# Optimization experiments

Hardware: AMD Instinct MI355X
Metric: run time of the kernel (lower is better)

Reference implementation:

```python
import jax, jax.numpy as jnp
import numpy as np
import math

B, NQ, NKV, D, H, KP = 4, 8192, 8192, 256, 8, 256
HD = D // H


def setup_inputs() -> dict:
    key = jax.random.key(0)
    ks = jax.random.split(key, 8)
    s = 1.0 / math.sqrt(D)
    return {
        "x1": jax.random.normal(ks[0], (B, NQ, D), dtype=jnp.float32),
        "x2": jax.random.normal(ks[1], (NKV, D), dtype=jnp.float32),
        "Wq": jax.random.normal(ks[2], (D, D), dtype=jnp.float32) * s,
        "Wk": jax.random.normal(ks[3], (D, D), dtype=jnp.float32) * s,
        "Wv": jax.random.normal(ks[4], (D, D), dtype=jnp.float32) * s,
        "Wo": jax.random.normal(ks[5], (D, D), dtype=jnp.float32) * s,
        "E": jax.random.normal(ks[6], (NKV, KP), dtype=jnp.float32) * (1.0 / math.sqrt(NKV)),
        "F": jax.random.normal(ks[7], (NKV, KP), dtype=jnp.float32) * (1.0 / math.sqrt(NKV)),
    }


def reference(x1, x2, Wq, Wk, Wv, Wo, E, F):
    # x1: [B, NQ, D] queries; x2: [NKV, D] shared cross-attention context
    q = x1 @ Wq                               # [B, NQ, D]
    k = x2 @ Wk                               # [NKV, D]
    v = x2 @ Wv                               # [NKV, D]
    # Linformer low-rank compression along the KV sequence axis
    k_low = jnp.einsum('nd,nk->kd', k, E)     # [KP, D]
    v_low = jnp.einsum('nd,nk->kd', v, F)     # [KP, D]
    qh = q.reshape(B, NQ, H, HD)
    kh = k_low.reshape(KP, H, HD)
    vh = v_low.reshape(KP, H, HD)
    scale = 1.0 / math.sqrt(HD)
    scores = jnp.einsum('bqhd,khd->bhqk', qh, kh) * scale  # [B, H, NQ, KP]
    attn = jax.nn.softmax(scores, axis=-1)
    out = jnp.einsum('bhqk,khd->bqhd', attn, vh)           # [B, NQ, H, HD]
    out = out.reshape(B, NQ, D)
    return out @ Wo
```

## Files before the change

kernel.cpp:

```cpp
#include <hip/hip_runtime.h>
#include <math.h>
#include <stdint.h>


typedef unsigned short ushort_t;
typedef __attribute__((ext_vector_type(8))) short bf16x8;
typedef __attribute__((ext_vector_type(8))) _Float16 f16x8;
typedef __attribute__((ext_vector_type(4))) float f32x4;

__device__ __forceinline__ f32x4 MFMA(bf16x8 a, bf16x8 b, f32x4 c) {
  return __builtin_amdgcn_mfma_f32_16x16x32_bf16(a, b, c, 0, 0, 0);
}
__device__ __forceinline__ f32x4 MFMA_H(f16x8 a, f16x8 b, f32x4 c) {
  return __builtin_amdgcn_mfma_f32_16x16x32_f16(a, b, c, 0, 0, 0);
}
__device__ __forceinline__ ushort_t f2bf(float x) {
  uint32_t u = __float_as_uint(x);
  u += 0x7fffu + ((u >> 16) & 1u);
  return (ushort_t)(u >> 16);
}
#define GLDS(gsrc, ldst)                                                    \
  __builtin_amdgcn_global_load_lds(                                         \
      (const __attribute__((address_space(1))) uint32_t*)(const void*)(gsrc), \
      (__attribute__((address_space(3))) uint32_t*)(void*)(ldst), 16, 0, 0)

#define STAGE_ROW(u) \
  (((((u) >> 2) ^ ((u) >> 4)) & 1) | (((u) >> 2) & 6) | (((u) >> 5) << 3))
#define STAGE_G(u) \
  ((((u) ^ ((u) >> 2) ^ ((u) >> 4)) & 1) | (((((u) >> 1) ^ ((u) >> 3)) & 1) << 1))

__global__ __launch_bounds__(256) void k_transpose(
    const float* __restrict__ x2, const float* __restrict__ E,
    const float* __restrict__ F, _Float16* __restrict__ xt) {
  __shared__ float tile[64][65];
  const int t = threadIdx.x;
  const int n0 = blockIdx.x * 64;
  const int c0 = blockIdx.y * 64;
  const int z = blockIdx.z;
  const float* __restrict__ src = (z == 0) ? x2 : (z == 1) ? E : F;
  _Float16* __restrict__ dst = xt + (size_t)z * 2097152;
  const int rr = t >> 4, cc = (t & 15) * 4;
#pragma unroll
  for (int i = 0; i < 4; ++i) {
    float4 v = *(const float4*)&src[(size_t)(n0 + rr + 16 * i) * 256 + c0 + cc];
    tile[cc + 0][rr + 16 * i] = v.x;
    tile[cc + 1][rr + 16 * i] = v.y;
    tile[cc + 2][rr + 16 * i] = v.z;
    tile[cc + 3][rr + 16 * i] = v.w;
  }
  __syncthreads();
#pragma unroll
  for (int rnd = 0; rnd < 2; ++rnd) {
    const int u = rnd * 256 + t;
    const int c = u >> 3, r0 = (u & 7) * 8;
    f16x8 h;
#pragma unroll
    for (int j = 0; j < 8; ++j) h[j] = (_Float16)tile[c][r0 + j];
    *(f16x8*)&dst[(size_t)(c0 + c) * 8192 + n0 + r0] = h;
  }
}

__global__ __launch_bounds__(256) void k_prep_w(
    const float* __restrict__ Wq, const float* __restrict__ Wk,
    const float* __restrict__ Wv, const float* __restrict__ Wo,
    ushort_t* __restrict__ wqt, ushort_t* __restrict__ wot,
    _Float16* __restrict__ wkt, _Float16* __restrict__ wvt) {
  const int id = blockIdx.x * 256 + threadIdx.x;
  const int task = blockIdx.y;
  const int n = id >> 8, k = id & 255;
  if (task == 0) wqt[id] = f2bf(Wq[k * 256 + n] * 0.25503488f);
  else if (task == 1) wot[id] = f2bf(Wo[k * 256 + n]);
  else if (task == 2) wkt[id] = (_Float16)Wk[k * 256 + n];
  else wvt[id] = (_Float16)Wv[k * 256 + n];
}

__global__ __launch_bounds__(256, 2) void k_etx2_mfma(
    const _Float16* __restrict__ xt, float* __restrict__ part) {
  __shared__ __align__(16) _Float16 ab[2][2][8192];
  const int t = threadIdx.x;
  const int ln = t & 63;
  const int wv = t >> 6;
  const int l15 = ln & 15, g = ln >> 4;
  const int wr = wv >> 1, wc = wv & 1;
  const int kp0 = (blockIdx.x >> 1) * 128;
  const int d0 = (blockIdx.x & 1) * 128;
  const int chunk = blockIdx.y;
  const int which = blockIdx.z;
  const int n0 = chunk * 256;
  const _Float16* __restrict__ A = xt + (size_t)(1 + which) * 2097152;
  const _Float16* __restrict__ B = xt;

  auto stage = [&](int buf, int ks) {
#pragma unroll
    for (int m = 0; m < 2; ++m)
#pragma unroll
      for (int rnd = 0; rnd < 4; ++rnd) {
        const int u = rnd * 256 + t;
        const int row = u >> 3;
        const int cb = (u & 7) << 4;
        const int csw = cb ^ ((row & 7) << 4);
        const _Float16* gs =
            (m ? B + (size_t)(d0 + row) * 8192 : A + (size_t)(kp0 + row) * 8192) +
            n0 + ks * 64 + (csw >> 1);
        GLDS(gs, (char*)&ab[buf][m][0] + (u & ~63) * 16);
      }
  };

  f32x4 acc[4][4];
#pragma unroll
  for (int i = 0; i < 4; ++i)
#pragma unroll
    for (int j = 0; j < 4; ++j) acc[i][j] = {0.f, 0.f, 0.f, 0.f};

  stage(0, 0);
  __syncthreads();
  for (int ks = 0; ks < 4; ++ks) {
    if (ks < 3) stage((ks + 1) & 1, ks + 1);
    const char* la = (const char*)&ab[ks & 1][0][0];
    const char* lb = (const char*)&ab[ks & 1][1][0];
#pragma unroll
    for (int kk = 0; kk < 2; ++kk) {
      f16x8 af[4], bf[4];
#pragma unroll
      for (int i = 0; i < 4; ++i) {
        const int ra = wr * 64 + i * 16 + l15;
        af[i] = *(const f16x8*)(la + ra * 128 +
                                ((kk * 64 + g * 16) ^ ((ra & 7) << 4)));
      }
#pragma unroll
      for (int j = 0; j < 4; ++j) {
        const int rb = wc * 64 + j * 16 + l15;
        bf[j] = *(const f16x8*)(lb + rb * 128 +
                                ((kk * 64 + g * 16) ^ ((rb & 7) << 4)));
      }
#pragma unroll
      for (int i = 0; i < 4; ++i)
#pragma unroll
        for (int j = 0; j < 4; ++j) acc[i][j] = MFMA_H(af[i], bf[j], acc[i][j]);
    }
    __syncthreads();
  }
  float* __restrict__ p = part + ((size_t)which * 32 + chunk) * 65536;
#pragma unroll
  for (int i = 0; i < 4; ++i)
#pragma unroll
    for (int j = 0; j < 4; ++j)
#pragma unroll
      for (int r = 0; r < 4; ++r)
        p[(size_t)(kp0 + wr * 64 + i * 16 + g * 4 + r) * 256 + d0 + wc * 64 +
          j * 16 + l15] = acc[i][j][r];
}

__global__ __launch_bounds__(256) void k_reduce_part(
    const float* __restrict__ part, _Float16* __restrict__ ghh) {
  const int oid = blockIdx.x * 256 + threadIdx.x;
  const int which = oid >> 16;
  const int base = oid & 65535;
  const float* __restrict__ p = part + (size_t)which * 32 * 65536 + base;
  float s = 0.f;
#pragma unroll
  for (int c = 0; c < 32; ++c) s += p[c * 65536];
  ghh[oid] = (_Float16)s;
}

__global__ __launch_bounds__(256, 4) void k_lowproj(
    const _Float16* __restrict__ ghh, const _Float16* __restrict__ wkt,
    const _Float16* __restrict__ wvt, float* __restrict__ kvlow) {
  __shared__ __align__(16) _Float16 wstage[2][4096];
  const int t = threadIdx.x;
  const int wv = t >> 6, ln = t & 63;
  const int l15 = ln & 15, g = ln >> 4;
  const int which = blockIdx.y;
  const size_t r0 = (size_t)blockIdx.x * 64;
  const _Float16* __restrict__ A = ghh + (size_t)which * 65536;
  const _Float16* __restrict__ W = which ? wvt : wkt;
  float* __restrict__ outp = kvlow + (size_t)which * 65536;

  auto stage = [&](int row0, int colu, int buf) {
#pragma unroll
    for (int rnd = 0; rnd < 2; ++rnd) {
      const int u = rnd * 256 + wv * 64 + ln;
      const int row = STAGE_ROW(u);
      const int gg = STAGE_G(u);
      GLDS(W + (size_t)(row0 + row) * 256 + colu + gg * 8,
           &wstage[buf][(rnd * 256 + wv * 64) * 8]);
    }
  };

  f32x4 yacc[16];
#pragma unroll
  for (int i = 0; i < 16; ++i) yacc[i] = {0.f, 0.f, 0.f, 0.f};
  stage(0, 0, 0);
  const _Float16* arow = A + (r0 + wv * 16 + l15) * 256;
  __syncthreads();
  for (int ci = 0; ci < 16; ++ci) {
    const int nh = ci & 1, ks = ci >> 1;
    if (ci < 15) stage(((ci + 1) & 1) * 128, ((ci + 1) >> 1) * 32, (ci + 1) & 1);
    f16x8 afrag = *(const f16x8*)(arow + ks * 32 + g * 8);
    const _Float16* cw = wstage[ci & 1];
#pragma unroll
    for (int tt = 0; tt < 8; ++tt) {
      f16x8 bfr = *(const f16x8*)&cw[((tt * 16 + l15) * 32 + g * 8) ^
                                     ((l15 & 7) << 3)];
      yacc[nh * 8 + tt] = MFMA_H(afrag, bfr, yacc[nh * 8 + tt]);
    }
    __syncthreads();
  }
#pragma unroll
  for (int tt = 0; tt < 16; ++tt)
#pragma unroll
    for (int r = 0; r < 4; ++r)
      outp[(r0 + wv * 16 + g * 4 + r) * 256 + tt * 16 + l15] = yacc[tt][r];
}

__global__ __launch_bounds__(256) void k_prep2(
    const float* __restrict__ kvlow, ushort_t* __restrict__ klowA,
    ushort_t* __restrict__ vtb) {
  const int id = blockIdx.x * 256 + threadIdx.x;
  if (blockIdx.y == 0) {
    const int h = id >> 13, kp = (id >> 5) & 255, d = id & 31;
    klowA[h * 8192 + (((kp << 5) | d) ^ ((kp & 7) << 3))] =
        f2bf(kvlow[kp * 256 + h * 32 + d]);
  } else {
    const int kl = id & 127, d = (id >> 7) & 31, kh = (id >> 12) & 1, h = id >> 13;
    vtb[(((h * 2 + kh) * 32 + d) << 7) + (kl ^ ((d & 7) << 3))] =
        f2bf(kvlow[65536 + (kh * 128 + kl) * 256 + h * 32 + d]);
  }
}

__global__ __launch_bounds__(256, 4) void k_qgemm(
    const float* __restrict__ x1, const ushort_t* __restrict__ wqt,
    ushort_t* __restrict__ Qf) {
  __shared__ __align__(16) char smem[32768];
  const int t = threadIdx.x;
  const int wv = t >> 6, ln = t & 63;
  const int l15 = ln & 15, g = ln >> 4;
  const size_t r0 = (size_t)blockIdx.x * 64;
  ushort_t* wstage = (ushort_t*)smem;

  auto stage = [&](int row0, int colu, int buf) {
#pragma unroll
    for (int rnd = 0; rnd < 2; ++rnd) {
      const int u = rnd * 256 + wv * 64 + ln;
      const int row = STAGE_ROW(u);
      const int gg = STAGE_G(u);
      GLDS(wqt + (size_t)(row0 + row) * 256 + colu + gg * 8,
           &wstage[buf * 4096 + (rnd * 256 + wv * 64) * 8]);
    }
  };

  f32x4 qacc[16];
#pragma unroll
  for (int i = 0; i < 16; ++i) qacc[i] = {0.f, 0.f, 0.f, 0.f};
  stage(0, 0, 0);
  const float* xrow = x1 + (r0 + wv * 16 + l15) * 256;
  float4 xa = *(const float4*)(xrow + g * 8);
  float4 xb = *(const float4*)(xrow + g * 8 + 4);
  __syncthreads();

  for (int ci = 0; ci < 16; ++ci) {
    const int nh = ci & 1;
    if (ci < 15) stage(((ci + 1) & 1) * 128, ((ci + 1) >> 1) * 32, (ci + 1) & 1);
    bf16x8 afrag;
    afrag[0] = (short)f2bf(xa.x); afrag[1] = (short)f2bf(xa.y);
    afrag[2] = (short)f2bf(xa.z); afrag[3] = (short)f2bf(xa.w);
    afrag[4] = (short)f2bf(xb.x); afrag[5] = (short)f2bf(xb.y);
    afrag[6] = (short)f2bf(xb.z); afrag[7] = (short)f2bf(xb.w);
    const ushort_t* cw = &wstage[(ci & 1) * 4096];
#pragma unroll
    for (int tt = 0; tt < 8; ++tt) {
      bf16x8 bfr = *(const bf16x8*)&cw[((tt * 16 + l15) * 32 + g * 8) ^
                                       ((l15 & 7) << 3)];
      qacc[nh * 8 + tt] = MFMA(afrag, bfr, qacc[nh * 8 + tt]);
    }
    if (nh == 1 && ci < 15) {
      int ks = (ci >> 1) + 1;
      xa = *(const float4*)(xrow + ks * 32 + g * 8);
      xb = *(const float4*)(xrow + ks * 32 + g * 8 + 4);
    }
    __syncthreads();
  }
  char* myq = smem + wv * 8192;
#pragma unroll
  for (int tt = 0; tt < 16; ++tt)
#pragma unroll
    for (int r = 0; r < 4; ++r) {
      const int gr = g * 4 + r;
      *(ushort_t*)(myq + gr * 512 + (((tt * 16 + l15) * 2) ^ ((gr & 7) << 4))) =
          f2bf(qacc[tt][r]);
    }
  __builtin_amdgcn_sched_barrier(0);
  const int rt = blockIdx.x * 4 + wv;
#pragma unroll
  for (int hh = 0; hh < 8; ++hh) {
    bf16x8 qf = *(const bf16x8*)(myq + l15 * 512 +
                                 ((hh * 64 + g * 16) ^ ((l15 & 7) << 4)));
    *(bf16x8*)&Qf[((size_t)(rt * 8 + hh) * 64 + ln) * 8] = qf;
  }
}

__global__ __launch_bounds__(512, 4) void k_attn(
    const ushort_t* __restrict__ Qf, const ushort_t* __restrict__ klowA,
    const ushort_t* __restrict__ vtb, ushort_t* __restrict__ O) {
  __shared__ __align__(16) ushort_t kv[16384];
  __shared__ __align__(16) uint32_t p_buf[8][320];
  __shared__ __align__(16) ushort_t o_sl[8][640];
  const int t = threadIdx.x;
  const int wv = t >> 6, ln = t & 63;
  const int l15 = ln & 15, g = ln >> 4;
  const int h = blockIdx.y;
  const size_t r0 = (size_t)blockIdx.x * 128;

  {
    const ushort_t* ksrc = klowA + h * 8192;
    const ushort_t* vsrc = vtb + h * 8192;
#pragma unroll
    for (int rnd = 0; rnd < 2; ++rnd) {
      const int ub = rnd * 512 + wv * 64;
      GLDS(ksrc + (ub + ln) * 8, &kv[ub * 8]);
    }
#pragma unroll
    for (int rnd = 0; rnd < 2; ++rnd) {
      const int ub = rnd * 512 + wv * 64;
      GLDS(vsrc + (ub + ln) * 8, &kv[8192 + ub * 8]);
    }
  }
  const int rt = blockIdx.x * 8 + wv;
  bf16x8 qfrag = *(const bf16x8*)&Qf[((size_t)(rt * 8 + h) * 64 + ln) * 8];
  __syncthreads();

  f32x4 s[16];
#pragma unroll
  for (int tt = 0; tt < 16; ++tt) {
    bf16x8 kfr = *(const bf16x8*)&kv[((tt * 16 + l15) * 32 + g * 8) ^
                                     ((l15 & 7) << 3)];
    f32x4 z = {0.f, 0.f, 0.f, 0.f};
    s[tt] = MFMA(kfr, qfrag, z);
  }
  float sum = 0.f;
  uint32_t pw[16][2];
#pragma unroll
  for (int tt = 0; tt < 16; ++tt) {
    float e0 = exp2f(s[tt][0]), e1 = exp2f(s[tt][1]);
    float e2 = exp2f(s[tt][2]), e3 = exp2f(s[tt][3]);
    sum += (e0 + e1) + (e2 + e3);
    pw[tt][0] = (uint32_t)f2bf(e0) | ((uint32_t)f2bf(e1) << 16);
    pw[tt][1] = (uint32_t)f2bf(e2) | ((uint32_t)f2bf(e3) << 16);
  }
  sum += __shfl_xor(sum, 16);
  sum += __shfl_xor(sum, 32);
  const float rinv = 1.0f / sum;
  float rv[4];
#pragma unroll
  for (int r = 0; r < 4; ++r) rv[r] = __shfl(rinv, g * 4 + r);

  f32x4 oacc[2];
  oacc[0] = {0.f, 0.f, 0.f, 0.f};
  oacc[1] = {0.f, 0.f, 0.f, 0.f};
  uint32_t* pbw = &p_buf[wv][l15 * 20];
#pragma unroll
  for (int kh = 0; kh < 2; ++kh) {
    const char* cv = (const char*)&kv[8192 + kh * 4096];
#pragma unroll
    for (int ksl = 0; ksl < 4; ++ksl) {
      const int ks = kh * 4 + ksl;
      pbw[2 * g + 0] = pw[2 * ks][0];
      pbw[2 * g + 1] = pw[2 * ks][1];
      pbw[8 + 2 * g + 0] = pw[2 * ks + 1][0];
      pbw[8 + 2 * g + 1] = pw[2 * ks + 1][1];
      __builtin_amdgcn_sched_barrier(0);
      bf16x8 pfr = *(const bf16x8*)&p_buf[wv][l15 * 20 + 4 * g];
#pragma unroll
      for (int nt = 0; nt < 2; ++nt) {
        bf16x8 vfr = *(const bf16x8*)(cv + (nt * 16 + l15) * 256 +
                                      ((ksl * 64 + g * 16) ^ ((l15 & 7) << 4)));
        oacc[nt] = MFMA(pfr, vfr, oacc[nt]);
      }
      __builtin_amdgcn_sched_barrier(0);
    }
  }
#pragma unroll
  for (int nt = 0; nt < 2; ++nt)
#pragma unroll
    for (int r = 0; r < 4; ++r)
      o_sl[wv][(g * 4 + r) * 40 + nt * 16 + l15] = f2bf(oacc[nt][r] * rv[r]);
  __builtin_amdgcn_sched_barrier(0);
  {
    const int qr = ln >> 2, d0 = (ln & 3) * 8;
    bf16x8 ov = *(const bf16x8*)&o_sl[wv][qr * 40 + d0];
    *(bf16x8*)&O[(r0 + wv * 16 + qr) * 256 + h * 32 + d0] = ov;
  }
}

__global__ __launch_bounds__(256, 4) void k_ogemm(
    const ushort_t* __restrict__ O, const ushort_t* __restrict__ wot,
    float* __restrict__ out) {
  __shared__ __align__(16) ushort_t wstage[2][4096];
  const int t = threadIdx.x;
  const int wv = t >> 6, ln = t & 63;
  const int l15 = ln & 15, g = ln >> 4;
  const size_t r0 = (size_t)blockIdx.x * 64;

  auto stage = [&](int row0, int colu, int buf) {
#pragma unroll
    for (int rnd = 0; rnd < 2; ++rnd) {
      const int u = rnd * 256 + wv * 64 + ln;
      const int row = STAGE_ROW(u);
      const int gg = STAGE_G(u);
      GLDS(wot + (size_t)(row0 + row) * 256 + colu + gg * 8,
           &wstage[buf][(rnd * 256 + wv * 64) * 8]);
    }
  };

  f32x4 yacc[16];
#pragma unroll
  for (int i = 0; i < 16; ++i) yacc[i] = {0.f, 0.f, 0.f, 0.f};
  stage(0, 0, 0);
  const ushort_t* arow = O + (r0 + wv * 16 + l15) * 256;
  __syncthreads();
  for (int ci = 0; ci < 16; ++ci) {
    const int nh = ci & 1, ks = ci >> 1;
    if (ci < 15) stage(((ci + 1) & 1) * 128, ((ci + 1) >> 1) * 32, (ci + 1) & 1);
    bf16x8 afrag = *(const bf16x8*)(arow + ks * 32 + g * 8);
    const ushort_t* cw = wstage[ci & 1];
#pragma unroll
    for (int tt = 0; tt < 8; ++tt) {
      bf16x8 bfr = *(const bf16x8*)&cw[((tt * 16 + l15) * 32 + g * 8) ^
                                       ((l15 & 7) << 3)];
      yacc[nh * 8 + tt] = MFMA(afrag, bfr, yacc[nh * 8 + tt]);
    }
    __syncthreads();
  }
#pragma unroll
  for (int tt = 0; tt < 16; ++tt)
#pragma unroll
    for (int r = 0; r < 4; ++r)
      out[(r0 + wv * 16 + g * 4 + r) * 256 + tt * 16 + l15] = yacc[tt][r];
}

extern "C" void kernel_launch(void* const* d_in, const int* in_sizes, int n_in,
                              void* d_out, int out_size, void* d_ws, size_t ws_size,
                              hipStream_t stream) {
  const float* x1 = (const float*)d_in[0];
  const float* x2 = (const float*)d_in[1];
  const float* Wq = (const float*)d_in[2];
  const float* Wk = (const float*)d_in[3];
  const float* Wv = (const float*)d_in[4];
  const float* Wo = (const float*)d_in[5];
  const float* E  = (const float*)d_in[6];
  const float* F  = (const float*)d_in[7];
  float* out = (float*)d_out;
  float* ws = (float*)d_ws;
  _Float16* ghh = (_Float16*)ws;
  float* kvlow = ws + 65536;
  ushort_t* wqt = (ushort_t*)(ws + 196608);
  ushort_t* wot = (ushort_t*)(ws + 229376);
  _Float16* wkt = (_Float16*)(ws + 262144);
  _Float16* wvt = (_Float16*)(ws + 294912);
  ushort_t* klowA = (ushort_t*)(ws + 327680);
  ushort_t* vtb = (ushort_t*)(ws + 360448);
  float* part = ws + 393216;
  ushort_t* Qf = (ushort_t*)(ws + 393216);
  _Float16* xt = (_Float16*)(ws + 4587520);
  ushort_t* O = (ushort_t*)(ws + 4587520);

  k_transpose<<<dim3(128, 4, 3), 256, 0, stream>>>(x2, E, F, xt);
  k_prep_w<<<dim3(256, 4), 256, 0, stream>>>(Wq, Wk, Wv, Wo, wqt, wot, wkt, wvt);
  k_etx2_mfma<<<dim3(4, 32, 2), 256, 0, stream>>>(xt, part);
  k_reduce_part<<<512, 256, 0, stream>>>(part, ghh);
  k_lowproj<<<dim3(4, 2), 256, 0, stream>>>(ghh, wkt, wvt, kvlow);
  k_prep2<<<dim3(256, 2), 256, 0, stream>>>(kvlow, klowA, vtb);
  k_qgemm<<<512, 256, 0, stream>>>(x1, wqt, Qf);
  k_attn<<<dim3(256, 8), 512, 0, stream>>>(Qf, klowA, vtb, O);
  k_ogemm<<<512, 256, 0, stream>>>(O, wot, out);
}
```

Baseline: 98.81 us.

## Merge prep kernels, co-schedule Q GEMM with E^T x2 GEMM, fuse low-proj repack

Merges the x2/E/F transpose and the weight transposes into one launch, and transposes the weights through LDS tiles for coalesced access. The Q projection and the E^T·x2 / F^T·x2 partial GEMMs now run as separate block ranges of a single kernel, so their work overlaps. The partial GEMM uses larger K chunks, which halves the reduction partials, but it loses double buffering. The low-rank projection writes the swizzled bf16 K/V layouts directly, removing the prep2 kernel and the fp32 intermediate. The attention kernel handles two query tiles per block. Fewer launches and overlapped independent work are the aim; the risk is slower per-block pipelining in the partial GEMM.

```diff
diff --git a/kernel.cpp b/kernel.cpp
--- a/kernel.cpp
+++ b/kernel.cpp
@@ -29,126 +29,215 @@
 #define STAGE_G(u) \
   ((((u) ^ ((u) >> 2) ^ ((u) >> 4)) & 1) | (((((u) >> 1) ^ ((u) >> 3)) & 1) << 1))
 
-__global__ __launch_bounds__(256) void k_transpose(
+__global__ __launch_bounds__(256) void k_prep_all(
     const float* __restrict__ x2, const float* __restrict__ E,
-    const float* __restrict__ F, _Float16* __restrict__ xt) {
+    const float* __restrict__ F, const float* __restrict__ Wq,
+    const float* __restrict__ Wk, const float* __restrict__ Wv,
+    const float* __restrict__ Wo, _Float16* __restrict__ xt,
+    ushort_t* __restrict__ wqt, ushort_t* __restrict__ wot,
+    _Float16* __restrict__ wkt, _Float16* __restrict__ wvt) {
   __shared__ float tile[64][65];
   const int t = threadIdx.x;
-  const int n0 = blockIdx.x * 64;
-  const int c0 = blockIdx.y * 64;
   const int z = blockIdx.z;
-  const float* __restrict__ src = (z == 0) ? x2 : (z == 1) ? E : F;
-  _Float16* __restrict__ dst = xt + (size_t)z * 2097152;
-  const int rr = t >> 4, cc = (t & 15) * 4;
-#pragma unroll
-  for (int i = 0; i < 4; ++i) {
-    float4 v = *(const float4*)&src[(size_t)(n0 + rr + 16 * i) * 256 + c0 + cc];
-    tile[cc + 0][rr + 16 * i] = v.x;
-    tile[cc + 1][rr + 16 * i] = v.y;
-    tile[cc + 2][rr + 16 * i] = v.z;
-    tile[cc + 3][rr + 16 * i] = v.w;
-  }
-  __syncthreads();
-#pragma unroll
-  for (int rnd = 0; rnd < 2; ++rnd) {
-    const int u = rnd * 256 + t;
-    const int c = u >> 3, r0 = (u & 7) * 8;
-    f16x8 h;
-#pragma unroll
-    for (int j = 0; j < 8; ++j) h[j] = (_Float16)tile[c][r0 + j];
-    *(f16x8*)&dst[(size_t)(c0 + c) * 8192 + n0 + r0] = h;
-  }
-}
-
-__global__ __launch_bounds__(256) void k_prep_w(
-    const float* __restrict__ Wq, const float* __restrict__ Wk,
-    const float* __restrict__ Wv, const float* __restrict__ Wo,
-    ushort_t* __restrict__ wqt, ushort_t* __restrict__ wot,
-    _Float16* __restrict__ wkt, _Float16* __restrict__ wvt) {
-  const int id = blockIdx.x * 256 + threadIdx.x;
-  const int task = blockIdx.y;
-  const int n = id >> 8, k = id & 255;
-  if (task == 0) wqt[id] = f2bf(Wq[k * 256 + n] * 0.25503488f);
-  else if (task == 1) wot[id] = f2bf(Wo[k * 256 + n]);
-  else if (task == 2) wkt[id] = (_Float16)Wk[k * 256 + n];
-  else wvt[id] = (_Float16)Wv[k * 256 + n];
-}
-
-__global__ __launch_bounds__(256, 2) void k_etx2_mfma(
-    const _Float16* __restrict__ xt, float* __restrict__ part) {
-  __shared__ __align__(16) _Float16 ab[2][2][8192];
+  if (z < 3) {
+    const int n0 = blockIdx.x * 64;
+    const int c0 = blockIdx.y * 64;
+    const float* __restrict__ src = (z == 0) ? x2 : (z == 1) ? E : F;
+    _Float16* __restrict__ dst = xt + (size_t)z * 2097152;
+    const int rr = t >> 4, cc = (t & 15) * 4;
+#pragma unroll
+    for (int i = 0; i < 4; ++i) {
+      float4 v = *(const float4*)&src[(size_t)(n0 + rr + 16 * i) * 256 + c0 + cc];
+      tile[cc + 0][rr + 16 * i] = v.x;
+      tile[cc + 1][rr + 16 * i] = v.y;
+      tile[cc + 2][rr + 16 * i] = v.z;
+      tile[cc + 3][rr + 16 * i] = v.w;
+    }
+    __syncthreads();
+#pragma unroll
+    for (int rnd = 0; rnd < 2; ++rnd) {
+      const int u = rnd * 256 + t;
+      const int c = u >> 3, r0 = (u & 7) * 8;
+      f16x8 h;
+#pragma unroll
+      for (int j = 0; j < 8; ++j) h[j] = (_Float16)tile[c][r0 + j];
+      *(f16x8*)&dst[(size_t)(c0 + c) * 8192 + n0 + r0] = h;
+    }
+  } else {
+    if (blockIdx.x >= 16) return;
+    const int m = blockIdx.y;
+    const float* __restrict__ src = (m == 0) ? Wq : (m == 1) ? Wo
+                                  : (m == 2) ? Wk : Wv;
+    const int tr = (blockIdx.x >> 2) * 64;
+    const int tc = (blockIdx.x & 3) * 64;
+    const int rr = t >> 4, cc = (t & 15) * 4;
+#pragma unroll
+    for (int i = 0; i < 4; ++i) {
+      float4 v = *(const float4*)&src[(size_t)(tr + rr + 16 * i) * 256 + tc + cc];
+      tile[cc + 0][rr + 16 * i] = v.x;
+      tile[cc + 1][rr + 16 * i] = v.y;
+      tile[cc + 2][rr + 16 * i] = v.z;
+      tile[cc + 3][rr + 16 * i] = v.w;
+    }
+    __syncthreads();
+#pragma unroll
+    for (int rnd = 0; rnd < 2; ++rnd) {
+      const int u = rnd * 256 + t;
+      const int nl = u >> 3, kl = (u & 7) * 8;
+      if (m < 2) {
+        const float sc = (m == 0) ? 0.25503488f : 1.0f;
+        bf16x8 hv;
+#pragma unroll
+        for (int j = 0; j < 8; ++j) hv[j] = (short)f2bf(tile[nl][kl + j] * sc);
+        ushort_t* dst = (m == 0) ? wqt : wot;
+        *(bf16x8*)&dst[(size_t)(tc + nl) * 256 + tr + kl] = hv;
+      } else {
+        f16x8 hv;
+#pragma unroll
+        for (int j = 0; j < 8; ++j) hv[j] = (_Float16)tile[nl][kl + j];
+        _Float16* dst = (m == 2) ? wkt : wvt;
+        *(f16x8*)&dst[(size_t)(tc + nl) * 256 + tr + kl] = hv;
+      }
+    }
+  }
+}
+
+__global__ __launch_bounds__(256, 3) void k_mega1(
+    const float* __restrict__ x1, const _Float16* __restrict__ xt,
+    const ushort_t* __restrict__ wqt, ushort_t* __restrict__ Qf,
+    float* __restrict__ part) {
+  __shared__ __align__(16) char smem[32768];
   const int t = threadIdx.x;
-  const int ln = t & 63;
-  const int wv = t >> 6;
+  const int wv = t >> 6, ln = t & 63;
   const int l15 = ln & 15, g = ln >> 4;
-  const int wr = wv >> 1, wc = wv & 1;
-  const int kp0 = (blockIdx.x >> 1) * 128;
-  const int d0 = (blockIdx.x & 1) * 128;
-  const int chunk = blockIdx.y;
-  const int which = blockIdx.z;
-  const int n0 = chunk * 256;
-  const _Float16* __restrict__ A = xt + (size_t)(1 + which) * 2097152;
-  const _Float16* __restrict__ B = xt;
-
-  auto stage = [&](int buf, int ks) {
-#pragma unroll
-    for (int m = 0; m < 2; ++m)
-#pragma unroll
-      for (int rnd = 0; rnd < 4; ++rnd) {
-        const int u = rnd * 256 + t;
-        const int row = u >> 3;
-        const int cb = (u & 7) << 4;
-        const int csw = cb ^ ((row & 7) << 4);
+
+  if (blockIdx.x < 512) {
+    ushort_t* wstage = (ushort_t*)smem;
+    const size_t r0 = (size_t)blockIdx.x * 64;
+    auto stage = [&](int row0, int colu, int buf) {
+#pragma unroll
+      for (int rnd = 0; rnd < 2; ++rnd) {
+        const int u = rnd * 256 + wv * 64 + ln;
+        const int row = STAGE_ROW(u);
+        const int gg = STAGE_G(u);
+        GLDS(wqt + (size_t)(row0 + row) * 256 + colu + gg * 8,
+             &wstage[(buf * 512 + rnd * 256 + wv * 64) * 8]);
+      }
+    };
+    f32x4 qacc[16];
+#pragma unroll
+    for (int i = 0; i < 16; ++i) qacc[i] = {0.f, 0.f, 0.f, 0.f};
+    stage(0, 0, 0);
+    const float* xrow = x1 + (r0 + wv * 16 + l15) * 256;
+    float4 xa = *(const float4*)(xrow + g * 8);
+    float4 xb = *(const float4*)(xrow + g * 8 + 4);
+    __syncthreads();
+    for (int ci = 0; ci < 16; ++ci) {
+      const int nh = ci & 1;
+      if (ci < 15) stage(((ci + 1) & 1) * 128, ((ci + 1) >> 1) * 32, (ci + 1) & 1);
+      bf16x8 afrag;
+      afrag[0] = (short)f2bf(xa.x); afrag[1] = (short)f2bf(xa.y);
+      afrag[2] = (short)f2bf(xa.z); afrag[3] = (short)f2bf(xa.w);
+      afrag[4] = (short)f2bf(xb.x); afrag[5] = (short)f2bf(xb.y);
+      afrag[6] = (short)f2bf(xb.z); afrag[7] = (short)f2bf(xb.w);
+      const ushort_t* cw = &wstage[(ci & 1) * 4096];
+#pragma unroll
+      for (int tt = 0; tt < 8; ++tt) {
+        bf16x8 bfr = *(const bf16x8*)&cw[((tt * 16 + l15) * 32 + g * 8) ^
+                                         ((l15 & 7) << 3)];
+        qacc[nh * 8 + tt] = MFMA(afrag, bfr, qacc[nh * 8 + tt]);
+      }
+      if (nh == 1 && ci < 15) {
+        int ks = (ci >> 1) + 1;
+        xa = *(const float4*)(xrow + ks * 32 + g * 8);
+        xb = *(const float4*)(xrow + ks * 32 + g * 8 + 4);
+      }
+      __syncthreads();
+    }
+    char* myq = smem + wv * 8192;
+#pragma unroll
+    for (int tt = 0; tt < 16; ++tt)
+#pragma unroll
+      for (int r = 0; r < 4; ++r) {
+        const int gr = g * 4 + r;
+        *(ushort_t*)(myq + gr * 512 + (((tt * 16 + l15) * 2) ^ ((gr & 7) << 4))) =
+            f2bf(qacc[tt][r]);
+      }
+    __builtin_amdgcn_sched_barrier(0);
+    const int rt = blockIdx.x * 4 + wv;
+#pragma unroll
+    for (int hh = 0; hh < 8; ++hh) {
+      bf16x8 qf = *(const bf16x8*)(myq + l15 * 512 +
+                                   ((hh * 64 + g * 16) ^ ((l15 & 7) << 4)));
+      *(bf16x8*)&Qf[((size_t)(rt * 8 + hh) * 64 + ln) * 8] = qf;
+    }
+  } else {
+    const int bid = blockIdx.x - 512;
+    const int which = bid & 1;
+    const int chunk = (bid >> 1) & 15;
+    const int quad = bid >> 5;
+    const int kp0 = (quad >> 1) * 128;
+    const int d0 = (quad & 1) * 128;
+    const int n0 = chunk * 512;
+    const _Float16* __restrict__ A = xt + (size_t)(1 + which) * 2097152;
+    const _Float16* __restrict__ B = xt;
+    const int wr = wv >> 1, wc = wv & 1;
+    f32x4 acc[4][4];
+#pragma unroll
+    for (int i = 0; i < 4; ++i)
+#pragma unroll
+      for (int j = 0; j < 4; ++j) acc[i][j] = {0.f, 0.f, 0.f, 0.f};
+
+    for (int ks = 0; ks < 8; ++ks) {
+#pragma unroll
+      for (int r8 = 0; r8 < 8; ++r8) {
+        const int u = r8 * 256 + t;
+        const int mm = u >> 10;
+        const int uu = u & 1023;
+        const int row = uu >> 3;
+        const int nsw = ((uu ^ row) & 7) << 3;
         const _Float16* gs =
-            (m ? B + (size_t)(d0 + row) * 8192 : A + (size_t)(kp0 + row) * 8192) +
-            n0 + ks * 64 + (csw >> 1);
-        GLDS(gs, (char*)&ab[buf][m][0] + (u & ~63) * 16);
-      }
-  };
-
-  f32x4 acc[4][4];
-#pragma unroll
-  for (int i = 0; i < 4; ++i)
-#pragma unroll
-    for (int j = 0; j < 4; ++j) acc[i][j] = {0.f, 0.f, 0.f, 0.f};
-
-  stage(0, 0);
-  __syncthreads();
-  for (int ks = 0; ks < 4; ++ks) {
-    if (ks < 3) stage((ks + 1) & 1, ks + 1);
-    const char* la = (const char*)&ab[ks & 1][0][0];
-    const char* lb = (const char*)&ab[ks & 1][1][0];
-#pragma unroll
-    for (int kk = 0; kk < 2; ++kk) {
-      f16x8 af[4], bf[4];
-#pragma unroll
-      for (int i = 0; i < 4; ++i) {
-        const int ra = wr * 64 + i * 16 + l15;
-        af[i] = *(const f16x8*)(la + ra * 128 +
-                                ((kk * 64 + g * 16) ^ ((ra & 7) << 4)));
-      }
-#pragma unroll
-      for (int j = 0; j < 4; ++j) {
-        const int rb = wc * 64 + j * 16 + l15;
-        bf[j] = *(const f16x8*)(lb + rb * 128 +
-                                ((kk * 64 + g * 16) ^ ((rb & 7) << 4)));
-      }
-#pragma unroll
-      for (int i = 0; i < 4; ++i)
-#pragma unroll
-        for (int j = 0; j < 4; ++j) acc[i][j] = MFMA_H(af[i], bf[j], acc[i][j]);
-    }
-    __syncthreads();
-  }
-  float* __restrict__ p = part + ((size_t)which * 32 + chunk) * 65536;
-#pragma unroll
-  for (int i = 0; i < 4; ++i)
-#pragma unroll
-    for (int j = 0; j < 4; ++j)
-#pragma unroll
-      for (int r = 0; r < 4; ++r)
-        p[(size_t)(kp0 + wr * 64 + i * 16 + g * 4 + r) * 256 + d0 + wc * 64 +
-          j * 16 + l15] = acc[i][j][r];
+            (mm ? B + (size_t)(d0 + row) * 8192
+                : A + (size_t)(kp0 + row) * 8192) +
+            n0 + ks * 64 + nsw;
+        GLDS(gs, smem + (u & ~63) * 16);
+      }
+      __syncthreads();
+      const char* la = smem;
+      const char* lb = smem + 16384;
+#pragma unroll
+      for (int kk = 0; kk < 2; ++kk) {
+        f16x8 af[4], bf[4];
+#pragma unroll
+        for (int i = 0; i < 4; ++i) {
+          const int ra = wr * 64 + i * 16 + l15;
+          af[i] = *(const f16x8*)(la + ra * 128 +
+                                  ((kk * 64 + g * 16) ^ ((ra & 7) << 4)));
+        }
+#pragma unroll
+        for (int j = 0; j < 4; ++j) {
+          const int rb = wc * 64 + j * 16 + l15;
+          bf[j] = *(const f16x8*)(lb + rb * 128 +
+                                  ((kk * 64 + g * 16) ^ ((rb & 7) << 4)));
+        }
+#pragma unroll
+        for (int i = 0; i < 4; ++i)
+#pragma unroll
+          for (int j = 0; j < 4; ++j)
+            acc[i][j] = MFMA_H(af[i], bf[j], acc[i][j]);
+      }
+      __syncthreads();
+    }
+    float* __restrict__ p = part + ((size_t)which * 16 + chunk) * 65536;
+#pragma unroll
+    for (int i = 0; i < 4; ++i)
+#pragma unroll
+      for (int j = 0; j < 4; ++j)
+#pragma unroll
+        for (int r = 0; r < 4; ++r)
+          p[(size_t)(kp0 + wr * 64 + i * 16 + g * 4 + r) * 256 + d0 + wc * 64 +
+            j * 16 + l15] = acc[i][j][r];
+  }
 }
 
 __global__ __launch_bounds__(256) void k_reduce_part(
@@ -156,25 +245,25 @@
   const int oid = blockIdx.x * 256 + threadIdx.x;
   const int which = oid >> 16;
   const int base = oid & 65535;
-  const float* __restrict__ p = part + (size_t)which * 32 * 65536 + base;
+  const float* __restrict__ p = part + (size_t)which * 16 * 65536 + base;
   float s = 0.f;
 #pragma unroll
-  for (int c = 0; c < 32; ++c) s += p[c * 65536];
+  for (int c = 0; c < 16; ++c) s += p[c * 65536];
   ghh[oid] = (_Float16)s;
 }
 
-__global__ __launch_bounds__(256, 4) void k_lowproj(
+__global__ __launch_bounds__(256, 4) void k_lowproj2(
     const _Float16* __restrict__ ghh, const _Float16* __restrict__ wkt,
-    const _Float16* __restrict__ wvt, float* __restrict__ kvlow) {
+    const _Float16* __restrict__ wvt, ushort_t* __restrict__ klowA,
+    ushort_t* __restrict__ vtb) {
   __shared__ __align__(16) _Float16 wstage[2][4096];
   const int t = threadIdx.x;
   const int wv = t >> 6, ln = t & 63;
   const int l15 = ln & 15, g = ln >> 4;
   const int which = blockIdx.y;
-  const size_t r0 = (size_t)blockIdx.x * 64;
+  const int r0 = blockIdx.x * 64;
   const _Float16* __restrict__ A = ghh + (size_t)which * 65536;
   const _Float16* __restrict__ W = which ? wvt : wkt;
-  float* __restrict__ outp = kvlow + (size_t)which * 65536;
 
   auto stage = [&](int row0, int colu, int buf) {
 #pragma unroll
@@ -191,7 +280,7 @@
 #pragma unroll
   for (int i = 0; i < 16; ++i) yacc[i] = {0.f, 0.f, 0.f, 0.f};
   stage(0, 0, 0);
-  const _Float16* arow = A + (r0 + wv * 16 + l15) * 256;
+  const _Float16* arow = A + (size_t)(r0 + wv * 16 + l15) * 256;
   __syncthreads();
   for (int ci = 0; ci < 16; ++ci) {
     const int nh = ci & 1, ks = ci >> 1;
@@ -209,94 +298,18 @@
 #pragma unroll
   for (int tt = 0; tt < 16; ++tt)
 #pragma unroll
-    for (int r = 0; r < 4; ++r)
-      outp[(r0 + wv * 16 + g * 4 + r) * 256 + tt * 16 + l15] = yacc[tt][r];
-}
-
-__global__ __launch_bounds__(256) void k_prep2(
-    const float* __restrict__ kvlow, ushort_t* __restrict__ klowA,
-    ushort_t* __restrict__ vtb) {
-  const int id = blockIdx.x * 256 + threadIdx.x;
-  if (blockIdx.y == 0) {
-    const int h = id >> 13, kp = (id >> 5) & 255, d = id & 31;
-    klowA[h * 8192 + (((kp << 5) | d) ^ ((kp & 7) << 3))] =
-        f2bf(kvlow[kp * 256 + h * 32 + d]);
-  } else {
-    const int kl = id & 127, d = (id >> 7) & 31, kh = (id >> 12) & 1, h = id >> 13;
-    vtb[(((h * 2 + kh) * 32 + d) << 7) + (kl ^ ((d & 7) << 3))] =
-        f2bf(kvlow[65536 + (kh * 128 + kl) * 256 + h * 32 + d]);
-  }
-}
-
-__global__ __launch_bounds__(256, 4) void k_qgemm(
-    const float* __restrict__ x1, const ushort_t* __restrict__ wqt,
-    ushort_t* __restrict__ Qf) {
-  __shared__ __align__(16) char smem[32768];
-  const int t = threadIdx.x;
-  const int wv = t >> 6, ln = t & 63;
-  const int l15 = ln & 15, g = ln >> 4;
-  const size_t r0 = (size_t)blockIdx.x * 64;
-  ushort_t* wstage = (ushort_t*)smem;
-
-  auto stage = [&](int row0, int colu, int buf) {
-#pragma unroll
-    for (int rnd = 0; rnd < 2; ++rnd) {
-      const int u = rnd * 256 + wv * 64 + ln;
-      const int row = STAGE_ROW(u);
-      const int gg = STAGE_G(u);
-      GLDS(wqt + (size_t)(row0 + row) * 256 + colu + gg * 8,
-           &wstage[buf * 4096 + (rnd * 256 + wv * 64) * 8]);
-    }
-  };
-
-  f32x4 qacc[16];
-#pragma unroll
-  for (int i = 0; i < 16; ++i) qacc[i] = {0.f, 0.f, 0.f, 0.f};
-  stage(0, 0, 0);
-  const float* xrow = x1 + (r0 + wv * 16 + l15) * 256;
-  float4 xa = *(const float4*)(xrow + g * 8);
-  float4 xb = *(const float4*)(xrow + g * 8 + 4);
-  __syncthreads();
-
-  for (int ci = 0; ci < 16; ++ci) {
-    const int nh = ci & 1;
-    if (ci < 15) stage(((ci + 1) & 1) * 128, ((ci + 1) >> 1) * 32, (ci + 1) & 1);
-    bf16x8 afrag;
-    afrag[0] = (short)f2bf(xa.x); afrag[1] = (short)f2bf(xa.y);
-    afrag[2] = (short)f2bf(xa.z); afrag[3] = (short)f2bf(xa.w);
-    afrag[4] = (short)f2bf(xb.x); afrag[5] = (short)f2bf(xb.y);
-    afrag[6] = (short)f2bf(xb.z); afrag[7] = (short)f2bf(xb.w);
-    const ushort_t* cw = &wstage[(ci & 1) * 4096];
-#pragma unroll
-    for (int tt = 0; tt < 8; ++tt) {
-      bf16x8 bfr = *(const bf16x8*)&cw[((tt * 16 + l15) * 32 + g * 8) ^
-                                       ((l15 & 7) << 3)];
-      qacc[nh * 8 + tt] = MFMA(afrag, bfr, qacc[nh * 8 + tt]);
-    }
-    if (nh == 1 && ci < 15) {
-      int ks = (ci >> 1) + 1;
-      xa = *(const float4*)(xrow + ks * 32 + g * 8);
-      xb = *(const float4*)(xrow + ks * 32 + g * 8 + 4);
-    }
-    __syncthreads();
-  }
-  char* myq = smem + wv * 8192;
-#pragma unroll
-  for (int tt = 0; tt < 16; ++tt)
-#pragma unroll
     for (int r = 0; r < 4; ++r) {
-      const int gr = g * 4 + r;
-      *(ushort_t*)(myq + gr * 512 + (((tt * 16 + l15) * 2) ^ ((gr & 7) << 4))) =
-          f2bf(qacc[tt][r]);
-    }
-  __builtin_amdgcn_sched_barrier(0);
-  const int rt = blockIdx.x * 4 + wv;
-#pragma unroll
-  for (int hh = 0; hh < 8; ++hh) {
-    bf16x8 qf = *(const bf16x8*)(myq + l15 * 512 +
-                                 ((hh * 64 + g * 16) ^ ((l15 & 7) << 4)));
-    *(bf16x8*)&Qf[((size_t)(rt * 8 + hh) * 64 + ln) * 8] = qf;
-  }
+      const int rowi = r0 + wv * 16 + g * 4 + r;
+      const int c = tt * 16 + l15;
+      const int hh = c >> 5, d = c & 31;
+      const ushort_t val = f2bf(yacc[tt][r]);
+      if (which == 0) {
+        klowA[(hh << 13) + ((((rowi & 255) << 5) | d) ^ ((rowi & 7) << 3))] = val;
+      } else {
+        const int kh = (rowi >> 7) & 1, kl = rowi & 127;
+        vtb[(((hh * 2 + kh) * 32 + d) << 7) + (kl ^ ((d & 7) << 3))] = val;
+      }
+    }
 }
 
 __global__ __launch_bounds__(512, 4) void k_attn(
@@ -309,7 +322,7 @@
   const int wv = t >> 6, ln = t & 63;
   const int l15 = ln & 15, g = ln >> 4;
   const int h = blockIdx.y;
-  const size_t r0 = (size_t)blockIdx.x * 128;
+  const size_t r0 = (size_t)blockIdx.x * 256;
 
   {
     const ushort_t* ksrc = klowA + h * 8192;
@@ -325,70 +338,76 @@
       GLDS(vsrc + (ub + ln) * 8, &kv[8192 + ub * 8]);
     }
   }
-  const int rt = blockIdx.x * 8 + wv;
-  bf16x8 qfrag = *(const bf16x8*)&Qf[((size_t)(rt * 8 + h) * 64 + ln) * 8];
+  const int rtb = blockIdx.x * 16 + wv;
+  bf16x8 qfA = *(const bf16x8*)&Qf[((size_t)(rtb * 8 + h) * 64 + ln) * 8];
+  bf16x8 qfB = *(const bf16x8*)&Qf[((size_t)((rtb + 8) * 8 + h) * 64 + ln) * 8];
   __syncthreads();
 
-  f32x4 s[16];
-#pragma unroll
-  for (int tt = 0; tt < 16; ++tt) {
-    bf16x8 kfr = *(const bf16x8*)&kv[((tt * 16 + l15) * 32 + g * 8) ^
-                                     ((l15 & 7) << 3)];
-    f32x4 z = {0.f, 0.f, 0.f, 0.f};
-    s[tt] = MFMA(kfr, qfrag, z);
-  }
-  float sum = 0.f;
-  uint32_t pw[16][2];
-#pragma unroll
-  for (int tt = 0; tt < 16; ++tt) {
-    float e0 = exp2f(s[tt][0]), e1 = exp2f(s[tt][1]);
-    float e2 = exp2f(s[tt][2]), e3 = exp2f(s[tt][3]);
-    sum += (e0 + e1) + (e2 + e3);
-    pw[tt][0] = (uint32_t)f2bf(e0) | ((uint32_t)f2bf(e1) << 16);
-    pw[tt][1] = (uint32_t)f2bf(e2) | ((uint32_t)f2bf(e3) << 16);
-  }
-  sum += __shfl_xor(sum, 16);
-  sum += __shfl_xor(sum, 32);
-  const float rinv = 1.0f / sum;
-  float rv[4];
-#pragma unroll
-  for (int r = 0; r < 4; ++r) rv[r] = __shfl(rinv, g * 4 + r);
-
-  f32x4 oacc[2];
-  oacc[0] = {0.f, 0.f, 0.f, 0.f};
-  oacc[1] = {0.f, 0.f, 0.f, 0.f};
-  uint32_t* pbw = &p_buf[wv][l15 * 20];
-#pragma unroll
-  for (int kh = 0; kh < 2; ++kh) {
-    const char* cv = (const char*)&kv[8192 + kh * 4096];
-#pragma unroll
-    for (int ksl = 0; ksl < 4; ++ksl) {
-      const int ks = kh * 4 + ksl;
-      pbw[2 * g + 0] = pw[2 * ks][0];
-      pbw[2 * g + 1] = pw[2 * ks][1];
-      pbw[8 + 2 * g + 0] = pw[2 * ks + 1][0];
-      pbw[8 + 2 * g + 1] = pw[2 * ks + 1][1];
-      __builtin_amdgcn_sched_barrier(0);
-      bf16x8 pfr = *(const bf16x8*)&p_buf[wv][l15 * 20 + 4 * g];
-#pragma unroll
-      for (int nt = 0; nt < 2; ++nt) {
-        bf16x8 vfr = *(const bf16x8*)(cv + (nt * 16 + l15) * 256 +
-                                      ((ksl * 64 + g * 16) ^ ((l15 & 7) << 4)));
-        oacc[nt] = MFMA(pfr, vfr, oacc[nt]);
-      }
-      __builtin_amdgcn_sched_barrier(0);
-    }
-  }
-#pragma unroll
-  for (int nt = 0; nt < 2; ++nt)
-#pragma unroll
-    for (int r = 0; r < 4; ++r)
-      o_sl[wv][(g * 4 + r) * 40 + nt * 16 + l15] = f2bf(oacc[nt][r] * rv[r]);
-  __builtin_amdgcn_sched_barrier(0);
-  {
-    const int qr = ln >> 2, d0 = (ln & 3) * 8;
-    bf16x8 ov = *(const bf16x8*)&o_sl[wv][qr * 40 + d0];
-    *(bf16x8*)&O[(r0 + wv * 16 + qr) * 256 + h * 32 + d0] = ov;
+#pragma unroll
+  for (int st = 0; st < 2; ++st) {
+    const bf16x8 qfrag = st ? qfB : qfA;
+    f32x4 s[16];
+#pragma unroll
+    for (int tt = 0; tt < 16; ++tt) {
+      bf16x8 kfr = *(const bf16x8*)&kv[((tt * 16 + l15) * 32 + g * 8) ^
+                                       ((l15 & 7) << 3)];
+      f32x4 z = {0.f, 0.f, 0.f, 0.f};
+      s[tt] = MFMA(kfr, qfrag, z);
+    }
+    float sum = 0.f;
+    uint32_t pw[16][2];
+#pragma unroll
+    for (int tt = 0; tt < 16; ++tt) {
+      float e0 = exp2f(s[tt][0]), e1 = exp2f(s[tt][1]);
+      float e2 = exp2f(s[tt][2]), e3 = exp2f(s[tt][3]);
+      sum += (e0 + e1) + (e2 + e3);
+      pw[tt][0] = (uint32_t)f2bf(e0) | ((uint32_t)f2bf(e1) << 16);
+      pw[tt][1] = (uint32_t)f2bf(e2) | ((uint32_t)f2bf(e3) << 16);
+    }
+    sum += __shfl_xor(sum, 16);
+    sum += __shfl_xor(sum, 32);
+    const float rinv = 1.0f / sum;
+    float rv[4];
+#pragma unroll
+    for (int r = 0; r < 4; ++r) rv[r] = __shfl(rinv, g * 4 + r);
+
+    f32x4 oacc[2];
+    oacc[0] = {0.f, 0.f, 0.f, 0.f};
+    oacc[1] = {0.f, 0.f, 0.f, 0.f};
+    uint32_t* pbw = &p_buf[wv][l15 * 20];
+#pragma unroll
+    for (int kh = 0; kh < 2; ++kh) {
+      const char* cv = (const char*)&kv[8192 + kh * 4096];
+#pragma unroll
+      for (int ksl = 0; ksl < 4; ++ksl) {
+        const int ks = kh * 4 + ksl;
+        pbw[2 * g + 0] = pw[2 * ks][0];
+        pbw[2 * g + 1] = pw[2 * ks][1];
+        pbw[8 + 2 * g + 0] = pw[2 * ks + 1][0];
+        pbw[8 + 2 * g + 1] = pw[2 * ks + 1][1];
+        __builtin_amdgcn_sched_barrier(0);
+        bf16x8 pfr = *(const bf16x8*)&p_buf[wv][l15 * 20 + 4 * g];
+#pragma unroll
+        for (int nt = 0; nt < 2; ++nt) {
+          bf16x8 vfr = *(const bf16x8*)(cv + (nt * 16 + l15) * 256 +
+                                        ((ksl * 64 + g * 16) ^ ((l15 & 7) << 4)));
+          oacc[nt] = MFMA(pfr, vfr, oacc[nt]);
+        }
+        __builtin_amdgcn_sched_barrier(0);
+      }
+    }
+#pragma unroll
+    for (int nt = 0; nt < 2; ++nt)
+#pragma unroll
+      for (int r = 0; r < 4; ++r)
+        o_sl[wv][(g * 4 + r) * 40 + nt * 16 + l15] = f2bf(oacc[nt][r] * rv[r]);
+    __builtin_amdgcn_sched_barrier(0);
+    {
+      const int qr = ln >> 2, d0 = (ln & 3) * 8;
+      bf16x8 ov = *(const bf16x8*)&o_sl[wv][qr * 40 + d0];
+      *(bf16x8*)&O[(r0 + st * 128 + wv * 16 + qr) * 256 + h * 32 + d0] = ov;
+    }
+    __builtin_amdgcn_sched_barrier(0);
   }
 }
 
@@ -452,25 +471,22 @@
   float* out = (float*)d_out;
   float* ws = (float*)d_ws;
   _Float16* ghh = (_Float16*)ws;
-  float* kvlow = ws + 65536;
-  ushort_t* wqt = (ushort_t*)(ws + 196608);
-  ushort_t* wot = (ushort_t*)(ws + 229376);
-  _Float16* wkt = (_Float16*)(ws + 262144);
-  _Float16* wvt = (_Float16*)(ws + 294912);
-  ushort_t* klowA = (ushort_t*)(ws + 327680);
-  ushort_t* vtb = (ushort_t*)(ws + 360448);
-  float* part = ws + 393216;
-  ushort_t* Qf = (ushort_t*)(ws + 393216);
-  _Float16* xt = (_Float16*)(ws + 4587520);
-  ushort_t* O = (ushort_t*)(ws + 4587520);
-
-  k_transpose<<<dim3(128, 4, 3), 256, 0, stream>>>(x2, E, F, xt);
-  k_prep_w<<<dim3(256, 4), 256, 0, stream>>>(Wq, Wk, Wv, Wo, wqt, wot, wkt, wvt);
-  k_etx2_mfma<<<dim3(4, 32, 2), 256, 0, stream>>>(xt, part);
+  ushort_t* wqt = (ushort_t*)(ws + 65536);
+  ushort_t* wot = (ushort_t*)(ws + 98304);
+  _Float16* wkt = (_Float16*)(ws + 131072);
+  _Float16* wvt = (_Float16*)(ws + 163840);
+  ushort_t* klowA = (ushort_t*)(ws + 196608);
+  ushort_t* vtb = (ushort_t*)(ws + 229376);
+  float* part = ws + 262144;
+  ushort_t* Qf = (ushort_t*)(ws + 2359296);
+  _Float16* xt = (_Float16*)(ws + 6553600);
+  ushort_t* O = (ushort_t*)(ws + 6553600);
+
+  k_prep_all<<<dim3(128, 4, 4), 256, 0, stream>>>(x2, E, F, Wq, Wk, Wv, Wo, xt,
+                                                  wqt, wot, wkt, wvt);
+  k_mega1<<<640, 256, 0, stream>>>(x1, xt, wqt, Qf, part);
   k_reduce_part<<<512, 256, 0, stream>>>(part, ghh);
-  k_lowproj<<<dim3(4, 2), 256, 0, stream>>>(ghh, wkt, wvt, kvlow);
-  k_prep2<<<dim3(256, 2), 256, 0, stream>>>(kvlow, klowA, vtb);
-  k_qgemm<<<512, 256, 0, stream>>>(x1, wqt, Qf);
-  k_attn<<<dim3(256, 8), 512, 0, stream>>>(Qf, klowA, vtb, O);
+  k_lowproj2<<<dim3(4, 2), 256, 0, stream>>>(ghh, wkt, wvt, klowA, vtb);
+  k_attn<<<dim3(128, 8), 512, 0, stream>>>(Qf, klowA, vtb, O);
   k_ogemm<<<512, 256, 0, stream>>>(O, wot, out);
 }
```

After: 90.03 us. 1.1x faster.
